# Kernel tuning notes

Measured on AMD Instinct MI355X. Metric: run time of the kernel, lower is better.

Reference implementation:

```python
import jax, jax.numpy as jnp
import numpy as np

NV = 6890   # SMPL vertex count (hard-coded in module)
NF = 13776  # SMPL face count
BATCH = 64


def _make_laplacian():
    # Mirrors LaplacianLoss.__init__: symmetric -1 adjacency from triangle
    # faces, diagonal = vertex degree, each row normalized by diag + 1e-8.
    rng = np.random.default_rng(0)
    faces = rng.integers(0, NV, size=(NF, 3))
    L = np.zeros((NV, NV), dtype=np.float32)
    L[faces[:, 0], faces[:, 1]] = -1
    L[faces[:, 1], faces[:, 0]] = -1
    L[faces[:, 1], faces[:, 2]] = -1
    L[faces[:, 2], faces[:, 1]] = -1
    L[faces[:, 2], faces[:, 0]] = -1
    L[faces[:, 0], faces[:, 2]] = -1
    r, c = np.diag_indices(NV)
    L[r, c] = -L.sum(1)
    L = L / (np.diag(L)[:, None] + 1e-8)
    return jnp.asarray(L)


def setup_inputs() -> dict:
    key = jax.random.key(0)
    x = jax.random.normal(key, (BATCH, NV, 3), dtype=jnp.float32)
    laplacian = _make_laplacian()
    return {"x": x, "laplacian": laplacian}


def reference(x, laplacian):
    # Dense Laplacian applied per batch: [v,w] x [b,w,d] -> [b,v,d]
    lx = jnp.einsum('vw,bwd->bvd', laplacian, x)
    # Squared norm over coordinate dim, then mean over (batch, vertices)
    # (average=False branch of the original module).
    return jnp.mean(jnp.sum(lx * lx, axis=2))
```

## Files before the change

kernel.cpp:

```cpp
#include <hip/hip_runtime.h>

#define NV    6890
#define NB    64
#define NCOL  192
#define NC4   48
#define MAIN4 1722
#define NITP  28
#define VCAP  640
#define SCALE (1.0f / (64.0f * 6890.0f))

__global__ __launch_bounds__(256) void transpose_x_kernel(
    const float* __restrict__ x, float* __restrict__ Xt) {
  int i = blockIdx.x * blockDim.x + threadIdx.x;
  const int total = NV * NCOL;
  if (i >= total) return;
  int n = i % NCOL;
  int w = i / NCOL;
  Xt[i] = x[(size_t)(n / 3) * (NV * 3) + (size_t)w * 3 + (n % 3)];
}

template <bool USE_XT, bool USE_PARTIALS>
__global__ __launch_bounds__(256) void lap_rows_wave_kernel(
    const float* __restrict__ L,
    const float* __restrict__ X,
    float* __restrict__ partials,
    float* __restrict__ out_atomic) {
  const int lane = threadIdx.x & 63;
  const int wv   = threadIdx.x >> 6;
  const int v    = blockIdx.x * 4 + wv;
  if (v >= NV) return;

  __shared__ float2 s_ent[4][VCAP];
  float2* __restrict__ se = s_ent[wv];

  const float* __restrict__ row = L + (size_t)v * NV;
  const int head     = (v & 1) ? 2 : 0;
  const int extraPos = head ? 0 : (NV - 2);
  const float4* __restrict__ m4 = (const float4*)(row + head);
  const unsigned long long lmask = (1ull << lane) - 1ull;

  const int n0 = lane, n1 = lane + 64, n2 = lane + 128;
  const size_t o0 = (size_t)(n0 / 3) * (NV * 3) + (n0 % 3);
  const size_t o1 = (size_t)(n1 / 3) * (NV * 3) + (n1 % 3);
  const size_t o2 = (size_t)(n2 / 3) * (NV * 3) + (n2 % 3);

  float4 acc = make_float4(0.f, 0.f, 0.f, 0.f);

  auto gather = [&](float val, int col) {
    if (USE_XT) {
      if (lane < NC4) {
        const float4 g = ((const float4*)X)[(size_t)col * NC4 + lane];
        acc.x = fmaf(val, g.x, acc.x);
        acc.y = fmaf(val, g.y, acc.y);
        acc.z = fmaf(val, g.z, acc.z);
        acc.w = fmaf(val, g.w, acc.w);
      }
    } else {
      const size_t cb = (size_t)col * 3;
      acc.x = fmaf(val, X[cb + o0], acc.x);
      acc.y = fmaf(val, X[cb + o1], acc.y);
      acc.z = fmaf(val, X[cb + o2], acc.z);
    }
  };

  int nnz = 0;
  auto push = [&](bool nz, float val, int col) {
    unsigned long long m = __ballot(nz);
    int pos = nnz + __popcll(m & lmask);
    if (nz && pos < VCAP) se[pos] = make_float2(val, __int_as_float(col));
    nnz += __popcll(m);
  };

  float4 buf[4];
  #pragma unroll
  for (int k = 0; k < 4; ++k) buf[k] = m4[k * 64 + lane];

  {
    const bool act = lane < 2;
    const float val = act ? row[extraPos + lane] : 0.f;
    push(act && val != 0.f, val, extraPos + lane);
  }

  #pragma unroll 4
  for (int it = 0; it < NITP; ++it) {
    const float4 f = buf[it & 3];
    const int i = it * 64 + lane;
    buf[it & 3] = m4[min((it + 4) * 64 + lane, MAIN4 - 1)];
    const bool act = i < MAIN4;
    const int cb = head + i * 4;
    push(act && f.x != 0.f, f.x, cb);
    push(act && f.y != 0.f, f.y, cb + 1);
    push(act && f.z != 0.f, f.z, cb + 2);
    push(act && f.w != 0.f, f.w, cb + 3);
  }

  if (nnz <= VCAP) {
    const int cnt = nnz;
    #pragma unroll 4
    for (int j = 0; j < cnt; ++j) {
      const float2 e = se[j];
      gather(e.x, __float_as_int(e.y));
    }
  } else {
    acc = make_float4(0.f, 0.f, 0.f, 0.f);
    auto walk = [&](unsigned long long m, float src, int col0, int stride) {
      while (m) {
        const int s = (int)__builtin_ctzll(m);
        m &= m - 1;
        const float val =
            __int_as_float(__builtin_amdgcn_readlane(__float_as_int(src), s));
        gather(val, col0 + s * stride);
      }
    };
    {
      const bool act = lane < 2;
      const float val = act ? row[extraPos + lane] : 0.f;
      walk(__ballot(act && val != 0.f), val, extraPos, 1);
    }
    for (int it = 0; it < 27; ++it) {
      const int i = it * 64 + lane;
      const bool act = i < MAIN4;
      float4 f = make_float4(0.f, 0.f, 0.f, 0.f);
      if (act) f = m4[i];
      const int cb = head + it * 256;
      walk(__ballot(act && f.x != 0.f), f.x, cb + 0, 4);
      walk(__ballot(act && f.y != 0.f), f.y, cb + 1, 4);
      walk(__ballot(act && f.z != 0.f), f.z, cb + 2, 4);
      walk(__ballot(act && f.w != 0.f), f.w, cb + 3, 4);
    }
  }

  float sq = fmaf(acc.x, acc.x,
             fmaf(acc.y, acc.y,
             fmaf(acc.z, acc.z, acc.w * acc.w)));
  #pragma unroll
  for (int o = 32; o > 0; o >>= 1) sq += __shfl_down(sq, o);
  if (lane == 0) {
    if (USE_PARTIALS) partials[v] = sq;
    else              atomicAdd(out_atomic, sq * SCALE);
  }
}

__global__ __launch_bounds__(256) void reduce_kernel(
    const float* __restrict__ p, float* __restrict__ out) {
  int tid = threadIdx.x;
  float a = 0.0f;
  for (int i = tid; i < NV; i += 256) a += p[i];
  #pragma unroll
  for (int o = 32; o > 0; o >>= 1) a += __shfl_down(a, o);
  __shared__ float s_w[4];
  if ((tid & 63) == 0) s_w[tid >> 6] = a;
  __syncthreads();
  if (tid == 0) out[0] = (s_w[0] + s_w[1] + s_w[2] + s_w[3]) * SCALE;
}

__global__ void zero_out_kernel(float* p) {
  if (threadIdx.x == 0 && blockIdx.x == 0) p[0] = 0.0f;
}

extern "C" void kernel_launch(void* const* d_in, const int* in_sizes, int n_in,
                              void* d_out, int out_size, void* d_ws, size_t ws_size,
                              hipStream_t stream) {
  const float* x = (const float*)d_in[0];
  const float* L = (const float*)d_in[1];
  float* out = (float*)d_out;

  const size_t xt_bytes   = (size_t)NV * NCOL * sizeof(float);
  const size_t part_bytes = (size_t)NV * sizeof(float);
  const int grid = (NV + 3) / 4;

  if (ws_size >= xt_bytes + part_bytes) {
    float* Xt       = (float*)d_ws;
    float* partials = (float*)((char*)d_ws + xt_bytes);
    const int total = NV * NCOL;
    transpose_x_kernel<<<(total + 255) / 256, 256, 0, stream>>>(x, Xt);
    lap_rows_wave_kernel<true, true><<<grid, 256, 0, stream>>>(L, Xt, partials, nullptr);
    reduce_kernel<<<1, 256, 0, stream>>>(partials, out);
  } else if (ws_size >= part_bytes) {
    float* partials = (float*)d_ws;
    lap_rows_wave_kernel<false, true><<<grid, 256, 0, stream>>>(L, x, partials, nullptr);
    reduce_kernel<<<1, 256, 0, stream>>>(partials, out);
  } else {
    zero_out_kernel<<<1, 64, 0, stream>>>(out);
    lap_rows_wave_kernel<false, false><<<grid, 256, 0, stream>>>(L, x, nullptr, out);
  }
}
```

Baseline: 58.12 us.

## Split Laplacian scan into compress and SpMM kernels, drop X transpose

Replaces the transpose-plus-fused kernel with a compress kernel and an SpMM kernel. The compress kernel scans each dense Laplacian row and writes its nonzeros (value, column) to a global per-row list capped at 64 entries, plus a count. The SpMM kernel loads that list once per wave, broadcasts each entry with readlane, and gathers x directly in its original layout without a transposed copy. This removes the transpose kernel and the shared-memory staging, at the cost of one extra launch and a global round-trip for the compressed entries. Rows with more than 64 nonzeros fall back to rescanning the dense row.

```diff
diff --git a/kernel.cpp b/kernel.cpp
--- a/kernel.cpp
+++ b/kernel.cpp
@@ -2,72 +2,31 @@
 
 #define NV    6890
 #define NB    64
-#define NCOL  192
-#define NC4   48
 #define MAIN4 1722
 #define NITP  28
-#define VCAP  640
+#define ECAP  64
 #define SCALE (1.0f / (64.0f * 6890.0f))
 
-__global__ __launch_bounds__(256) void transpose_x_kernel(
-    const float* __restrict__ x, float* __restrict__ Xt) {
-  int i = blockIdx.x * blockDim.x + threadIdx.x;
-  const int total = NV * NCOL;
-  if (i >= total) return;
-  int n = i % NCOL;
-  int w = i / NCOL;
-  Xt[i] = x[(size_t)(n / 3) * (NV * 3) + (size_t)w * 3 + (n % 3)];
-}
-
-template <bool USE_XT, bool USE_PARTIALS>
-__global__ __launch_bounds__(256) void lap_rows_wave_kernel(
-    const float* __restrict__ L,
-    const float* __restrict__ X,
-    float* __restrict__ partials,
-    float* __restrict__ out_atomic) {
+__global__ __launch_bounds__(256) void compress_kernel(
+    const float* __restrict__ L, float2* __restrict__ ent,
+    int* __restrict__ cnt) {
   const int lane = threadIdx.x & 63;
   const int wv   = threadIdx.x >> 6;
   const int v    = blockIdx.x * 4 + wv;
   if (v >= NV) return;
-
-  __shared__ float2 s_ent[4][VCAP];
-  float2* __restrict__ se = s_ent[wv];
 
   const float* __restrict__ row = L + (size_t)v * NV;
   const int head     = (v & 1) ? 2 : 0;
   const int extraPos = head ? 0 : (NV - 2);
   const float4* __restrict__ m4 = (const float4*)(row + head);
   const unsigned long long lmask = (1ull << lane) - 1ull;
-
-  const int n0 = lane, n1 = lane + 64, n2 = lane + 128;
-  const size_t o0 = (size_t)(n0 / 3) * (NV * 3) + (n0 % 3);
-  const size_t o1 = (size_t)(n1 / 3) * (NV * 3) + (n1 % 3);
-  const size_t o2 = (size_t)(n2 / 3) * (NV * 3) + (n2 % 3);
-
-  float4 acc = make_float4(0.f, 0.f, 0.f, 0.f);
-
-  auto gather = [&](float val, int col) {
-    if (USE_XT) {
-      if (lane < NC4) {
-        const float4 g = ((const float4*)X)[(size_t)col * NC4 + lane];
-        acc.x = fmaf(val, g.x, acc.x);
-        acc.y = fmaf(val, g.y, acc.y);
-        acc.z = fmaf(val, g.z, acc.z);
-        acc.w = fmaf(val, g.w, acc.w);
-      }
-    } else {
-      const size_t cb = (size_t)col * 3;
-      acc.x = fmaf(val, X[cb + o0], acc.x);
-      acc.y = fmaf(val, X[cb + o1], acc.y);
-      acc.z = fmaf(val, X[cb + o2], acc.z);
-    }
-  };
+  float2* __restrict__ re = ent + (size_t)v * ECAP;
 
   int nnz = 0;
   auto push = [&](bool nz, float val, int col) {
     unsigned long long m = __ballot(nz);
     int pos = nnz + __popcll(m & lmask);
-    if (nz && pos < VCAP) se[pos] = make_float2(val, __int_as_float(col));
+    if (nz && pos < ECAP) re[pos] = make_float2(val, __int_as_float(col));
     nnz += __popcll(m);
   };
 
@@ -93,23 +52,55 @@
     push(act && f.z != 0.f, f.z, cb + 2);
     push(act && f.w != 0.f, f.w, cb + 3);
   }
-
-  if (nnz <= VCAP) {
-    const int cnt = nnz;
-    #pragma unroll 4
-    for (int j = 0; j < cnt; ++j) {
-      const float2 e = se[j];
-      gather(e.x, __float_as_int(e.y));
+  if (lane == 0) cnt[v] = nnz;
+}
+
+template <bool USE_PARTIALS>
+__global__ __launch_bounds__(256) void spmm_kernel(
+    const float* __restrict__ L, const float* __restrict__ x,
+    const float2* __restrict__ ent, const int* __restrict__ cnt,
+    float* __restrict__ partials, float* __restrict__ out_atomic) {
+  const int lane = threadIdx.x & 63;
+  const int wv   = threadIdx.x >> 6;
+  const int v    = blockIdx.x * 4 + wv;
+  if (v >= NV) return;
+
+  const int n0 = lane, n1 = lane + 64, n2 = lane + 128;
+  const int o0 = (n0 / 3) * (NV * 3) + (n0 % 3);
+  const int o1 = (n1 / 3) * (NV * 3) + (n1 % 3);
+  const int o2 = (n2 / 3) * (NV * 3) + (n2 % 3);
+
+  float a0 = 0.f, a1 = 0.f, a2 = 0.f;
+  const int c = cnt[v];
+
+  if (c <= ECAP) {
+    const float2 e = (lane < c) ? ent[(size_t)v * ECAP + lane]
+                                : make_float2(0.f, 0.f);
+    #pragma unroll 2
+    for (int j = 0; j < c; ++j) {
+      const float val =
+          __int_as_float(__builtin_amdgcn_readlane(__float_as_int(e.x), j));
+      const int col = __builtin_amdgcn_readlane(__float_as_int(e.y), j);
+      const int cb = col * 3;
+      a0 = fmaf(val, x[cb + o0], a0);
+      a1 = fmaf(val, x[cb + o1], a1);
+      a2 = fmaf(val, x[cb + o2], a2);
     }
   } else {
-    acc = make_float4(0.f, 0.f, 0.f, 0.f);
+    const float* __restrict__ row = L + (size_t)v * NV;
+    const int head     = (v & 1) ? 2 : 0;
+    const int extraPos = head ? 0 : (NV - 2);
+    const float4* __restrict__ m4 = (const float4*)(row + head);
     auto walk = [&](unsigned long long m, float src, int col0, int stride) {
       while (m) {
         const int s = (int)__builtin_ctzll(m);
         m &= m - 1;
         const float val =
             __int_as_float(__builtin_amdgcn_readlane(__float_as_int(src), s));
-        gather(val, col0 + s * stride);
+        const int cb = (col0 + s * stride) * 3;
+        a0 = fmaf(val, x[cb + o0], a0);
+        a1 = fmaf(val, x[cb + o1], a1);
+        a2 = fmaf(val, x[cb + o2], a2);
       }
     };
     {
@@ -130,9 +121,65 @@
     }
   }
 
-  float sq = fmaf(acc.x, acc.x,
-             fmaf(acc.y, acc.y,
-             fmaf(acc.z, acc.z, acc.w * acc.w)));
+  float sq = fmaf(a0, a0, fmaf(a1, a1, a2 * a2));
+  #pragma unroll
+  for (int o = 32; o > 0; o >>= 1) sq += __shfl_down(sq, o);
+  if (lane == 0) {
+    if (USE_PARTIALS) partials[v] = sq;
+    else              atomicAdd(out_atomic, sq * SCALE);
+  }
+}
+
+template <bool USE_PARTIALS>
+__global__ __launch_bounds__(256) void lap_fused_kernel(
+    const float* __restrict__ L, const float* __restrict__ x,
+    float* __restrict__ partials, float* __restrict__ out_atomic) {
+  const int lane = threadIdx.x & 63;
+  const int wv   = threadIdx.x >> 6;
+  const int v    = blockIdx.x * 4 + wv;
+  if (v >= NV) return;
+
+  const float* __restrict__ row = L + (size_t)v * NV;
+  const int head     = (v & 1) ? 2 : 0;
+  const int extraPos = head ? 0 : (NV - 2);
+  const float4* __restrict__ m4 = (const float4*)(row + head);
+
+  const int n0 = lane, n1 = lane + 64, n2 = lane + 128;
+  const int o0 = (n0 / 3) * (NV * 3) + (n0 % 3);
+  const int o1 = (n1 / 3) * (NV * 3) + (n1 % 3);
+  const int o2 = (n2 / 3) * (NV * 3) + (n2 % 3);
+
+  float a0 = 0.f, a1 = 0.f, a2 = 0.f;
+  auto walk = [&](unsigned long long m, float src, int col0, int stride) {
+    while (m) {
+      const int s = (int)__builtin_ctzll(m);
+      m &= m - 1;
+      const float val =
+          __int_as_float(__builtin_amdgcn_readlane(__float_as_int(src), s));
+      const int cb = (col0 + s * stride) * 3;
+      a0 = fmaf(val, x[cb + o0], a0);
+      a1 = fmaf(val, x[cb + o1], a1);
+      a2 = fmaf(val, x[cb + o2], a2);
+    }
+  };
+  {
+    const bool act = lane < 2;
+    const float val = act ? row[extraPos + lane] : 0.f;
+    walk(__ballot(act && val != 0.f), val, extraPos, 1);
+  }
+  for (int it = 0; it < 27; ++it) {
+    const int i = it * 64 + lane;
+    const bool act = i < MAIN4;
+    float4 f = make_float4(0.f, 0.f, 0.f, 0.f);
+    if (act) f = m4[i];
+    const int cb = head + it * 256;
+    walk(__ballot(act && f.x != 0.f), f.x, cb + 0, 4);
+    walk(__ballot(act && f.y != 0.f), f.y, cb + 1, 4);
+    walk(__ballot(act && f.z != 0.f), f.z, cb + 2, 4);
+    walk(__ballot(act && f.w != 0.f), f.w, cb + 3, 4);
+  }
+
+  float sq = fmaf(a0, a0, fmaf(a1, a1, a2 * a2));
   #pragma unroll
   for (int o = 32; o > 0; o >>= 1) sq += __shfl_down(sq, o);
   if (lane == 0) {
@@ -165,23 +212,24 @@
   const float* L = (const float*)d_in[1];
   float* out = (float*)d_out;
 
-  const size_t xt_bytes   = (size_t)NV * NCOL * sizeof(float);
+  const size_t ent_bytes  = (size_t)NV * ECAP * sizeof(float2);
+  const size_t cnt_bytes  = (size_t)NV * sizeof(int);
   const size_t part_bytes = (size_t)NV * sizeof(float);
   const int grid = (NV + 3) / 4;
 
-  if (ws_size >= xt_bytes + part_bytes) {
-    float* Xt       = (float*)d_ws;
-    float* partials = (float*)((char*)d_ws + xt_bytes);
-    const int total = NV * NCOL;
-    transpose_x_kernel<<<(total + 255) / 256, 256, 0, stream>>>(x, Xt);
-    lap_rows_wave_kernel<true, true><<<grid, 256, 0, stream>>>(L, Xt, partials, nullptr);
+  if (ws_size >= ent_bytes + cnt_bytes + part_bytes) {
+    float2* ent     = (float2*)d_ws;
+    int*    cnt     = (int*)((char*)d_ws + ent_bytes);
+    float*  partials = (float*)((char*)d_ws + ent_bytes + cnt_bytes);
+    compress_kernel<<<grid, 256, 0, stream>>>(L, ent, cnt);
+    spmm_kernel<true><<<grid, 256, 0, stream>>>(L, x, ent, cnt, partials, nullptr);
     reduce_kernel<<<1, 256, 0, stream>>>(partials, out);
   } else if (ws_size >= part_bytes) {
     float* partials = (float*)d_ws;
-    lap_rows_wave_kernel<false, true><<<grid, 256, 0, stream>>>(L, x, partials, nullptr);
+    lap_fused_kernel<true><<<grid, 256, 0, stream>>>(L, x, partials, nullptr);
     reduce_kernel<<<1, 256, 0, stream>>>(partials, out);
   } else {
     zero_out_kernel<<<1, 64, 0, stream>>>(out);
-    lap_rows_wave_kernel<false, false><<<grid, 256, 0, stream>>>(L, x, nullptr, out);
-  }
-}
+    lap_fused_kernel<false><<<grid, 256, 0, stream>>>(L, x, nullptr, out);
+  }
+}
```

Result: slower. 82.70 us (+42.3%).

## Compact nonzero float4 chunks with one ballot per chunk and deeper prefetch

Applied to the files above, without the earlier changes.

The row scan now issues one ballot per float4 chunk instead of one per scalar, storing whole nonzero chunks plus a base column in shared memory, and the gather then skips zero components. Prefetch depth rises from 4 to 8 float4 loads, and blocks shrink to 2 waves so more blocks fit per CU. The aim is to cut the ballot and popcount overhead of scanning the dense 6890-wide rows and to keep more loads in flight. The smaller capacity of 128 chunks may push dense rows onto the slow fallback path. The no-transpose paths move to a separate walk-based kernel.

```diff
diff --git a/kernel.cpp b/kernel.cpp
--- a/kernel.cpp
+++ b/kernel.cpp
@@ -5,8 +5,9 @@
 #define NCOL  192
 #define NC4   48
 #define MAIN4 1722
-#define NITP  28
-#define VCAP  640
+#define NITP  32
+#define DEPTH 8
+#define VCAP  128
 #define SCALE (1.0f / (64.0f * 6890.0f))
 
 __global__ __launch_bounds__(256) void transpose_x_kernel(
@@ -19,19 +20,21 @@
   Xt[i] = x[(size_t)(n / 3) * (NV * 3) + (size_t)w * 3 + (n % 3)];
 }
 
-template <bool USE_XT, bool USE_PARTIALS>
-__global__ __launch_bounds__(256) void lap_rows_wave_kernel(
+template <bool USE_PARTIALS>
+__global__ __launch_bounds__(128) void lap_rows_wave_kernel(
     const float* __restrict__ L,
-    const float* __restrict__ X,
+    const float* __restrict__ Xt,
     float* __restrict__ partials,
     float* __restrict__ out_atomic) {
   const int lane = threadIdx.x & 63;
   const int wv   = threadIdx.x >> 6;
-  const int v    = blockIdx.x * 4 + wv;
+  const int v    = blockIdx.x * 2 + wv;
   if (v >= NV) return;
 
-  __shared__ float2 s_ent[4][VCAP];
-  float2* __restrict__ se = s_ent[wv];
+  __shared__ float4 s_c4[2][VCAP];
+  __shared__ int    s_cb[2][VCAP];
+  float4* __restrict__ sc4 = s_c4[wv];
+  int*    __restrict__ scb = s_cb[wv];
 
   const float* __restrict__ row = L + (size_t)v * NV;
   const int head     = (v & 1) ? 2 : 0;
@@ -39,67 +42,60 @@
   const float4* __restrict__ m4 = (const float4*)(row + head);
   const unsigned long long lmask = (1ull << lane) - 1ull;
 
-  const int n0 = lane, n1 = lane + 64, n2 = lane + 128;
-  const size_t o0 = (size_t)(n0 / 3) * (NV * 3) + (n0 % 3);
-  const size_t o1 = (size_t)(n1 / 3) * (NV * 3) + (n1 % 3);
-  const size_t o2 = (size_t)(n2 / 3) * (NV * 3) + (n2 % 3);
+  int nnz = 0;
+
+  auto pushc = [&](unsigned long long m, float4 f, int colbase) {
+    if (m) {
+      const int pos = nnz + __popcll(m & lmask);
+      const bool mine = (m >> lane) & 1ull;
+      if (mine && pos < VCAP) { sc4[pos] = f; scb[pos] = colbase; }
+      nnz += __popcll(m);
+    }
+  };
+
+  {
+    const float h0 = row[extraPos];
+    const float h1 = row[extraPos + 1];
+    const bool nz = (lane == 0) &&
+                    ((__float_as_uint(h0) | __float_as_uint(h1)) != 0u);
+    pushc(__ballot(nz), make_float4(h0, h1, 0.f, 0.f), extraPos);
+  }
+
+  float4 buf[DEPTH];
+  #pragma unroll
+  for (int k = 0; k < DEPTH; ++k) buf[k] = m4[k * 64 + lane];
+
+  #pragma unroll DEPTH
+  for (int it = 0; it < NITP; ++it) {
+    const float4 f = buf[it & (DEPTH - 1)];
+    buf[it & (DEPTH - 1)] = m4[min((it + DEPTH) * 64 + lane, MAIN4 - 1)];
+    const int i = it * 64 + lane;
+    const unsigned u = __float_as_uint(f.x) | __float_as_uint(f.y) |
+                       __float_as_uint(f.z) | __float_as_uint(f.w);
+    pushc(__ballot((i < MAIN4) && (u != 0u)), f, head + i * 4);
+  }
 
   float4 acc = make_float4(0.f, 0.f, 0.f, 0.f);
 
-  auto gather = [&](float val, int col) {
-    if (USE_XT) {
-      if (lane < NC4) {
-        const float4 g = ((const float4*)X)[(size_t)col * NC4 + lane];
-        acc.x = fmaf(val, g.x, acc.x);
-        acc.y = fmaf(val, g.y, acc.y);
-        acc.z = fmaf(val, g.z, acc.z);
-        acc.w = fmaf(val, g.w, acc.w);
-      }
-    } else {
-      const size_t cb = (size_t)col * 3;
-      acc.x = fmaf(val, X[cb + o0], acc.x);
-      acc.y = fmaf(val, X[cb + o1], acc.y);
-      acc.z = fmaf(val, X[cb + o2], acc.z);
+  auto gatherc = [&](float val, int col) {
+    if (lane < NC4) {
+      const float4 g = ((const float4*)Xt)[(size_t)col * NC4 + lane];
+      acc.x = fmaf(val, g.x, acc.x);
+      acc.y = fmaf(val, g.y, acc.y);
+      acc.z = fmaf(val, g.z, acc.z);
+      acc.w = fmaf(val, g.w, acc.w);
     }
   };
-
-  int nnz = 0;
-  auto push = [&](bool nz, float val, int col) {
-    unsigned long long m = __ballot(nz);
-    int pos = nnz + __popcll(m & lmask);
-    if (nz && pos < VCAP) se[pos] = make_float2(val, __int_as_float(col));
-    nnz += __popcll(m);
-  };
-
-  float4 buf[4];
-  #pragma unroll
-  for (int k = 0; k < 4; ++k) buf[k] = m4[k * 64 + lane];
-
-  {
-    const bool act = lane < 2;
-    const float val = act ? row[extraPos + lane] : 0.f;
-    push(act && val != 0.f, val, extraPos + lane);
-  }
-
-  #pragma unroll 4
-  for (int it = 0; it < NITP; ++it) {
-    const float4 f = buf[it & 3];
-    const int i = it * 64 + lane;
-    buf[it & 3] = m4[min((it + 4) * 64 + lane, MAIN4 - 1)];
-    const bool act = i < MAIN4;
-    const int cb = head + i * 4;
-    push(act && f.x != 0.f, f.x, cb);
-    push(act && f.y != 0.f, f.y, cb + 1);
-    push(act && f.z != 0.f, f.z, cb + 2);
-    push(act && f.w != 0.f, f.w, cb + 3);
-  }
 
   if (nnz <= VCAP) {
     const int cnt = nnz;
-    #pragma unroll 4
     for (int j = 0; j < cnt; ++j) {
-      const float2 e = se[j];
-      gather(e.x, __float_as_int(e.y));
+      const float4 c = sc4[j];
+      const int   cb = scb[j];
+      if (__float_as_uint(c.x)) gatherc(c.x, cb);
+      if (__float_as_uint(c.y)) gatherc(c.y, cb + 1);
+      if (__float_as_uint(c.z)) gatherc(c.z, cb + 2);
+      if (__float_as_uint(c.w)) gatherc(c.w, cb + 3);
     }
   } else {
     acc = make_float4(0.f, 0.f, 0.f, 0.f);
@@ -109,7 +105,7 @@
         m &= m - 1;
         const float val =
             __int_as_float(__builtin_amdgcn_readlane(__float_as_int(src), s));
-        gather(val, col0 + s * stride);
+        gatherc(val, col0 + s * stride);
       }
     };
     {
@@ -141,6 +137,64 @@
   }
 }
 
+template <bool USE_PARTIALS>
+__global__ __launch_bounds__(256) void lap_fused_kernel(
+    const float* __restrict__ L, const float* __restrict__ x,
+    float* __restrict__ partials, float* __restrict__ out_atomic) {
+  const int lane = threadIdx.x & 63;
+  const int wv   = threadIdx.x >> 6;
+  const int v    = blockIdx.x * 4 + wv;
+  if (v >= NV) return;
+
+  const float* __restrict__ row = L + (size_t)v * NV;
+  const int head     = (v & 1) ? 2 : 0;
+  const int extraPos = head ? 0 : (NV - 2);
+  const float4* __restrict__ m4 = (const float4*)(row + head);
+
+  const int n0 = lane, n1 = lane + 64, n2 = lane + 128;
+  const int o0 = (n0 / 3) * (NV * 3) + (n0 % 3);
+  const int o1 = (n1 / 3) * (NV * 3) + (n1 % 3);
+  const int o2 = (n2 / 3) * (NV * 3) + (n2 % 3);
+
+  float a0 = 0.f, a1 = 0.f, a2 = 0.f;
+  auto walk = [&](unsigned long long m, float src, int col0, int stride) {
+    while (m) {
+      const int s = (int)__builtin_ctzll(m);
+      m &= m - 1;
+      const float val =
+          __int_as_float(__builtin_amdgcn_readlane(__float_as_int(src), s));
+      const int cb = (col0 + s * stride) * 3;
+      a0 = fmaf(val, x[cb + o0], a0);
+      a1 = fmaf(val, x[cb + o1], a1);
+      a2 = fmaf(val, x[cb + o2], a2);
+    }
+  };
+  {
+    const bool act = lane < 2;
+    const float val = act ? row[extraPos + lane] : 0.f;
+    walk(__ballot(act && val != 0.f), val, extraPos, 1);
+  }
+  for (int it = 0; it < 27; ++it) {
+    const int i = it * 64 + lane;
+    const bool act = i < MAIN4;
+    float4 f = make_float4(0.f, 0.f, 0.f, 0.f);
+    if (act) f = m4[i];
+    const int cb = head + it * 256;
+    walk(__ballot(act && f.x != 0.f), f.x, cb + 0, 4);
+    walk(__ballot(act && f.y != 0.f), f.y, cb + 1, 4);
+    walk(__ballot(act && f.z != 0.f), f.z, cb + 2, 4);
+    walk(__ballot(act && f.w != 0.f), f.w, cb + 3, 4);
+  }
+
+  float sq = fmaf(a0, a0, fmaf(a1, a1, a2 * a2));
+  #pragma unroll
+  for (int o = 32; o > 0; o >>= 1) sq += __shfl_down(sq, o);
+  if (lane == 0) {
+    if (USE_PARTIALS) partials[v] = sq;
+    else              atomicAdd(out_atomic, sq * SCALE);
+  }
+}
+
 __global__ __launch_bounds__(256) void reduce_kernel(
     const float* __restrict__ p, float* __restrict__ out) {
   int tid = threadIdx.x;
@@ -167,21 +221,20 @@
 
   const size_t xt_bytes   = (size_t)NV * NCOL * sizeof(float);
   const size_t part_bytes = (size_t)NV * sizeof(float);
-  const int grid = (NV + 3) / 4;
 
   if (ws_size >= xt_bytes + part_bytes) {
     float* Xt       = (float*)d_ws;
     float* partials = (float*)((char*)d_ws + xt_bytes);
     const int total = NV * NCOL;
     transpose_x_kernel<<<(total + 255) / 256, 256, 0, stream>>>(x, Xt);
-    lap_rows_wave_kernel<true, true><<<grid, 256, 0, stream>>>(L, Xt, partials, nullptr);
+    lap_rows_wave_kernel<true><<<(NV + 1) / 2, 128, 0, stream>>>(L, Xt, partials, nullptr);
     reduce_kernel<<<1, 256, 0, stream>>>(partials, out);
   } else if (ws_size >= part_bytes) {
     float* partials = (float*)d_ws;
-    lap_rows_wave_kernel<false, true><<<grid, 256, 0, stream>>>(L, x, partials, nullptr);
+    lap_fused_kernel<true><<<(NV + 3) / 4, 256, 0, stream>>>(L, x, partials, nullptr);
     reduce_kernel<<<1, 256, 0, stream>>>(partials, out);
   } else {
     zero_out_kernel<<<1, 64, 0, stream>>>(out);
-    lap_rows_wave_kernel<false, false><<<grid, 256, 0, stream>>>(L, x, nullptr, out);
-  }
-}
+    lap_fused_kernel<false><<<(NV + 3) / 4, 256, 0, stream>>>(L, x, nullptr, out);
+  }
+}
```

Result: slower. 60.95 us (+4.9%).
